# Kernel optimization log

Hardware: AMD Instinct MI355X
Metric: run time of the kernel (lower is better)

The kernel has to match this reference:

```python
import jax, jax.numpy as jnp
import numpy as np

N_HEADS = 16

def setup_inputs() -> dict:
    key = jax.random.key(0)
    k1, k2, k3, k4, k5 = jax.random.split(key, 5)
    B, T, C = 4, 2048, 1024
    x = jax.random.normal(k1, (B, T, C), dtype=jnp.float32)
    W_attn = jax.random.normal(k2, (C, 3 * C), dtype=jnp.float32) * 0.02
    b_attn = jnp.zeros((3 * C,), dtype=jnp.float32)
    W_proj = jax.random.normal(k3, (C, C), dtype=jnp.float32) * 0.02
    b_proj = jnp.zeros((C,), dtype=jnp.float32)
    return {"x": x, "W_attn": W_attn, "b_attn": b_attn, "W_proj": W_proj, "b_proj": b_proj}

def reference(x, W_attn, b_attn, W_proj, b_proj):
    B, T, C = x.shape
    H = N_HEADS
    hd = C // H
    qkv = x @ W_attn + b_attn                      # [B,T,3C]
    q, k, v = jnp.split(qkv, 3, axis=-1)
    q = q.reshape(B, T, H, hd)
    k = k.reshape(B, T, H, hd)
    v = v.reshape(B, T, H, hd)
    scale = 0.1 / jnp.sqrt(jnp.float32(hd))
    scores = jnp.einsum('bqhd,bkhd->bhqk', q, k) * scale   # [B,H,T,T]
    causal = jnp.tril(jnp.ones((T, T), dtype=bool))
    scores = jnp.where(causal[None, None], scores, jnp.float32(-jnp.inf))
    attn = jax.nn.softmax(scores, axis=-1)
    y = jnp.einsum('bhqk,bkhd->bqhd', attn, v).reshape(B, T, C)
    return y @ W_proj + b_proj
```

## Files before the change

kernel.cpp:

```cpp
#include <hip/hip_runtime.h>

typedef __attribute__((ext_vector_type(8))) __bf16 bf16x8;
typedef __attribute__((ext_vector_type(4))) float  f32x4;
typedef __attribute__((ext_vector_type(4))) short  short4v;
typedef __attribute__((ext_vector_type(4))) float  float4v;

#define MFMA16(a,b,c) __builtin_amdgcn_mfma_f32_16x16x32_bf16((a),(b),(c),0,0,0)

__device__ __forceinline__ short f2bf(float f){
    unsigned int u = __builtin_bit_cast(unsigned int, f);
    u += 0x7fffu + ((u >> 16) & 1u);
    return (short)(u >> 16);
}

typedef __attribute__((address_space(1))) void gvoid;
typedef __attribute__((address_space(3))) void lvoid;
__device__ __forceinline__ void async_copy16(const void* g, void* l){
    __builtin_amdgcn_global_load_lds(
        (gvoid*)(unsigned long long)g,
        (lvoid*)(unsigned int)(unsigned long long)l,
        16, 0, 0);
}

#define BATCH 4
#define SEQ   2048
#define CDIM  1024
#define NH    16
#define HD    64
#define BT    8192
#define QSCALE 0.0125f
#define L2E 1.44269504088896340736f

__global__ __launch_bounds__(256) void cvt_x(const float* __restrict__ x,
                                             short* __restrict__ xb){
    int idx = blockIdx.x * 256 + threadIdx.x;
    const float* s = x + (size_t)idx * 8;
    float4v a = *(const float4v*)(s);
    float4v b = *(const float4v*)(s + 4);
    short4v lo, hi;
#pragma unroll
    for (int j = 0; j < 4; ++j){ lo[j] = f2bf(a[j]); hi[j] = f2bf(b[j]); }
    short4v* d = (short4v*)(xb + (size_t)idx * 8);
    d[0] = lo; d[1] = hi;
}

__global__ __launch_bounds__(256) void wtrans(const float* __restrict__ W,
                                              short* __restrict__ Wt,
                                              int K, int N){
    __shared__ __align__(16) short lds[64 * 80];
    int tid = threadIdx.x;
    int n0 = blockIdx.x * 64, k0 = blockIdx.y * 64;
#pragma unroll
    for (int it = 0; it < 4; ++it){
        int idx = it * 256 + tid;
        int r = idx >> 4, c4 = (idx & 15) << 2;
        float4v w = *(const float4v*)(W + (size_t)(k0 + r) * N + n0 + c4);
        short4v h4;
#pragma unroll
        for (int j = 0; j < 4; ++j) h4[j] = f2bf(w[j]);
        *(short4v*)(&lds[r * 80 + c4]) = h4;
    }
    __syncthreads();
#pragma unroll
    for (int it = 0; it < 2; ++it){
        int idx = it * 256 + tid;
        int nl = idx >> 3, k8 = (idx & 7) << 3;
        short4v o0, o1;
#pragma unroll
        for (int j = 0; j < 4; ++j){
            o0[j] = lds[(k8 + j) * 80 + nl];
            o1[j] = lds[(k8 + 4 + j) * 80 + nl];
        }
        short4v* d = (short4v*)(Wt + (size_t)(n0 + nl) * K + k0 + k8);
        d[0] = o0; d[1] = o1;
    }
}

#define BM 128
#define BN 128
#define BK 32
#define KDIM 1024

__global__ __launch_bounds__(256) void qkv_gemm(const short* __restrict__ A,
                                                const short* __restrict__ Bt,
                                                const float* __restrict__ bias,
                                                short* __restrict__ q,
                                                short* __restrict__ k,
                                                short* __restrict__ v){
    __shared__ __align__(16) short As[2][BM * BK];
    __shared__ __align__(16) short Bs[2][BM * BK];
    const int tid = threadIdx.x;
    const int bn = blockIdx.x, bm = blockIdx.y;
    const int lane = tid & 63, wid = tid >> 6;
    const int wr = wid >> 1, wc = wid & 1;
    const int li = lane & 15, g = lane >> 4;
    const int arow0 = bm * BM, brow0 = bn * BN;

    f32x4 acc[4][4];
#pragma unroll
    for (int i = 0; i < 4; ++i)
#pragma unroll
        for (int j = 0; j < 4; ++j) acc[i][j] = f32x4{0.f,0.f,0.f,0.f};

    auto stage = [&](int buf, int kt){
        const short* ga = A  + (size_t)arow0 * KDIM + kt * BK;
        const short* gb = Bt + (size_t)brow0 * KDIM + kt * BK;
#pragma unroll
        for (int h = 0; h < 2; ++h){
            int f = h * 256 + tid;
            int row = f >> 2, kc = (f & 3) << 3;
            async_copy16(ga + (size_t)row * KDIM + kc, &As[buf][f << 3]);
            async_copy16(gb + (size_t)row * KDIM + kc, &Bs[buf][f << 3]);
        }
    };

    stage(0, 0);
    __syncthreads();
    int buf = 0;
    const int KT = KDIM / BK;
    for (int kt = 0; kt < KT; ++kt){
        if (kt + 1 < KT) stage(buf ^ 1, kt + 1);
        bf16x8 af[4], bfr[4];
#pragma unroll
        for (int mi = 0; mi < 4; ++mi)
            af[mi] = *(const bf16x8*)(&As[buf][(wr*64 + mi*16 + li) * BK + g*8]);
#pragma unroll
        for (int ni = 0; ni < 4; ++ni)
            bfr[ni] = *(const bf16x8*)(&Bs[buf][(wc*64 + ni*16 + li) * BK + g*8]);
#pragma unroll
        for (int mi = 0; mi < 4; ++mi)
#pragma unroll
            for (int ni = 0; ni < 4; ++ni)
                acc[mi][ni] = MFMA16(af[mi], bfr[ni], acc[mi][ni]);
        __syncthreads();
        buf ^= 1;
    }

    const int sec = bn >> 3;
    const int h   = ((bn & 7) << 1) | wc;
    short* dst = (sec == 0) ? q : ((sec == 1) ? k : v);
    const float mul = (sec == 0) ? QSCALE : 1.0f;
#pragma unroll
    for (int ni = 0; ni < 4; ++ni){
        int d = ni * 16 + li;
        float bb = bias[bn * 128 + wc * 64 + d];
#pragma unroll
        for (int mi = 0; mi < 4; ++mi){
#pragma unroll
            for (int r = 0; r < 4; ++r){
                int row = arow0 + wr * 64 + mi * 16 + g * 4 + r;
                int b_ = row >> 11, t = row & 2047;
                float val = (acc[mi][ni][r] + bb) * mul;
                dst[(((size_t)(b_ * NH + h)) * SEQ + t) * HD + d] = f2bf(val);
            }
        }
    }
}

__global__ __launch_bounds__(256) void proj_gemm(const short* __restrict__ A,
                                                 const short* __restrict__ Bt,
                                                 const float* __restrict__ bias,
                                                 float* __restrict__ out){
    __shared__ __align__(16) short As[2][BM * BK];
    __shared__ __align__(16) short Bs[2][BM * BK];
    const int tid = threadIdx.x;
    const int bn = blockIdx.x, bm = blockIdx.y;
    const int lane = tid & 63, wid = tid >> 6;
    const int wr = wid >> 1, wc = wid & 1;
    const int li = lane & 15, g = lane >> 4;
    const int arow0 = bm * BM, brow0 = bn * BN;

    f32x4 acc[4][4];
#pragma unroll
    for (int i = 0; i < 4; ++i)
#pragma unroll
        for (int j = 0; j < 4; ++j) acc[i][j] = f32x4{0.f,0.f,0.f,0.f};

    auto stage = [&](int buf, int kt){
        const short* ga = A  + (size_t)arow0 * KDIM + kt * BK;
        const short* gb = Bt + (size_t)brow0 * KDIM + kt * BK;
#pragma unroll
        for (int h = 0; h < 2; ++h){
            int f = h * 256 + tid;
            int row = f >> 2, kc = (f & 3) << 3;
            async_copy16(ga + (size_t)row * KDIM + kc, &As[buf][f << 3]);
            async_copy16(gb + (size_t)row * KDIM + kc, &Bs[buf][f << 3]);
        }
    };

    stage(0, 0);
    __syncthreads();
    int buf = 0;
    const int KT = KDIM / BK;
    for (int kt = 0; kt < KT; ++kt){
        if (kt + 1 < KT) stage(buf ^ 1, kt + 1);
        bf16x8 af[4], bfr[4];
#pragma unroll
        for (int mi = 0; mi < 4; ++mi)
            af[mi] = *(const bf16x8*)(&As[buf][(wr*64 + mi*16 + li) * BK + g*8]);
#pragma unroll
        for (int ni = 0; ni < 4; ++ni)
            bfr[ni] = *(const bf16x8*)(&Bs[buf][(wc*64 + ni*16 + li) * BK + g*8]);
#pragma unroll
        for (int mi = 0; mi < 4; ++mi)
#pragma unroll
            for (int ni = 0; ni < 4; ++ni)
                acc[mi][ni] = MFMA16(af[mi], bfr[ni], acc[mi][ni]);
        __syncthreads();
        buf ^= 1;
    }

#pragma unroll
    for (int ni = 0; ni < 4; ++ni){
        int c = brow0 + wc * 64 + ni * 16 + li;
        float bb = bias[c];
#pragma unroll
        for (int mi = 0; mi < 4; ++mi){
#pragma unroll
            for (int r = 0; r < 4; ++r){
                int row = arow0 + wr * 64 + mi * 16 + g * 4 + r;
                out[(size_t)row * CDIM + c] = acc[mi][ni][r] + bb;
            }
        }
    }
}

__global__ __launch_bounds__(256) void vtrans(const short* __restrict__ v,
                                              short* __restrict__ vt){
    __shared__ __align__(16) short lds[64 * 80];
    int tid = threadIdx.x;
    int t0 = blockIdx.x * 64;
    int bh = blockIdx.y;
    const short* src = v + ((size_t)bh * SEQ + t0) * HD;
#pragma unroll
    for (int it = 0; it < 2; ++it){
        int idx = it * 256 + tid;
        int r = idx >> 3, c8 = (idx & 7) << 3;
        *(bf16x8*)(&lds[r * 80 + c8]) = *(const bf16x8*)(src + (size_t)r * HD + c8);
    }
    __syncthreads();
    short* dst = vt + (size_t)bh * HD * SEQ + t0;
#pragma unroll
    for (int it = 0; it < 2; ++it){
        int idx = it * 256 + tid;
        int dl = idx >> 3, t8 = (idx & 7) << 3;
        short4v o0, o1;
#pragma unroll
        for (int j = 0; j < 4; ++j){
            o0[j] = lds[(t8 + j) * 80 + dl];
            o1[j] = lds[(t8 + 4 + j) * 80 + dl];
        }
        short4v* d = (short4v*)(dst + (size_t)dl * SEQ + t8);
        d[0] = o0; d[1] = o1;
    }
}

__global__ __launch_bounds__(256) void attn_kernel(const short* __restrict__ q,
                                                   const short* __restrict__ kk,
                                                   const short* __restrict__ vt,
                                                   short* __restrict__ y){
    __shared__ __align__(16) char kvs[2][2][8192];
    __shared__ __align__(16) char psm[4 * 2048];
    const int tid = threadIdx.x;
    const int qt = 31 - blockIdx.x;
    const int bh = blockIdx.y;
    const int lane = tid & 63, wid = tid >> 6;
    const int li = lane & 15, g = lane >> 4;
    const int iglob = qt * 64 + wid * 16 + li;

    const short* qp = q + ((size_t)bh * SEQ + iglob) * HD;
    bf16x8 qf0 = *(const bf16x8*)(qp + g * 8);
    bf16x8 qf1 = *(const bf16x8*)(qp + 32 + g * 8);

    char* pbase = psm + wid * 2048 + li * 128;
    const int sw = (li & 7) << 4;

    f32x4 acc[4];
#pragma unroll
    for (int df = 0; df < 4; ++df) acc[df] = f32x4{0.f,0.f,0.f,0.f};
    float m = -3e38f, l = 0.f;

    const short* kbp = kk + (size_t)bh * SEQ * HD;
    const short* vbp = vt + (size_t)bh * HD * SEQ;

    const int c0 = (wid * 2) * 64 + lane;
    const int r0 = c0 >> 3, sg0 = (c0 & 7) ^ (r0 & 7);
    const int c1 = c0 + 64;
    const int r1 = c1 >> 3, sg1 = (c1 & 7) ^ (r1 & 7);

    auto stage = [&](int b, int kt2){
        const int kb2 = kt2 * 64;
        const short* kg = kbp + (size_t)kb2 * HD;
        const short* vg = vbp + kb2;
        char* kd = kvs[b][0];
        char* vd = kvs[b][1];
        async_copy16(kg + r0 * HD + sg0 * 8, kd + c0 * 16);
        async_copy16(kg + r1 * HD + sg1 * 8, kd + c1 * 16);
        async_copy16(vg + (size_t)r0 * SEQ + sg0 * 8, vd + c0 * 16);
        async_copy16(vg + (size_t)r1 * SEQ + sg1 * 8, vd + c1 * 16);
    };

    stage(0, 0);
    asm volatile("s_waitcnt vmcnt(0)" ::: "memory");
    __builtin_amdgcn_s_barrier();
    int buf = 0;
    for (int kt = 0; kt <= qt; ++kt){
        const int kb = kt * 64;
        if (kt < qt) stage(buf ^ 1, kt + 1);

        const char* Kb = kvs[buf][0];
        const char* Vb = kvs[buf][1];

        f32x4 st[4];
#pragma unroll
        for (int kf = 0; kf < 4; ++kf) st[kf] = f32x4{0.f,0.f,0.f,0.f};
#pragma unroll
        for (int kf = 0; kf < 4; ++kf){
            int r = kf * 16 + li;
            bf16x8 k0 = *(const bf16x8*)(Kb + r * 128 + ((g ^ (r & 7)) << 4));
            bf16x8 k1 = *(const bf16x8*)(Kb + r * 128 + (((g + 4) ^ (r & 7)) << 4));
            st[kf] = MFMA16(k0, qf0, st[kf]);
            st[kf] = MFMA16(k1, qf1, st[kf]);
        }
        if (kt == qt){
#pragma unroll
            for (int kf = 0; kf < 4; ++kf)
#pragma unroll
                for (int r = 0; r < 4; ++r)
                    if (kb + kf * 16 + g * 4 + r > iglob) st[kf][r] = -3e38f;
        }
        float pm = -3e38f;
#pragma unroll
        for (int kf = 0; kf < 4; ++kf)
#pragma unroll
            for (int r = 0; r < 4; ++r) pm = fmaxf(pm, st[kf][r]);
        pm = fmaxf(pm, __shfl_xor(pm, 16, 64));
        pm = fmaxf(pm, __shfl_xor(pm, 32, 64));
        float mnew = fmaxf(m, pm);
        float alpha = __builtin_amdgcn_exp2f((m - mnew) * L2E);
        float rs = 0.f;
#pragma unroll
        for (int kf = 0; kf < 4; ++kf){
            short4v pk;
#pragma unroll
            for (int r = 0; r < 4; ++r){
                float p = __builtin_amdgcn_exp2f((st[kf][r] - mnew) * L2E);
                rs += p;
                pk[r] = f2bf(p);
            }
            *(short4v*)(pbase + (((kf << 5) + (g << 3)) ^ sw)) = pk;
        }
        rs += __shfl_xor(rs, 16, 64);
        rs += __shfl_xor(rs, 32, 64);
        l = l * alpha + rs;
        m = mnew;
#pragma unroll
        for (int df = 0; df < 4; ++df) acc[df] *= alpha;

        bf16x8 pb0 = *(const bf16x8*)(pbase + (((g << 4)) ^ sw));
        bf16x8 pb1 = *(const bf16x8*)(pbase + ((64 + (g << 4)) ^ sw));
#pragma unroll
        for (int df = 0; df < 4; ++df){
            int d = df * 16 + li;
            bf16x8 v0 = *(const bf16x8*)(Vb + d * 128 + ((g ^ (d & 7)) << 4));
            bf16x8 v1 = *(const bf16x8*)(Vb + d * 128 + (((g + 4) ^ (d & 7)) << 4));
            acc[df] = MFMA16(v0, pb0, acc[df]);
            acc[df] = MFMA16(v1, pb1, acc[df]);
        }

        asm volatile("s_waitcnt vmcnt(0)" ::: "memory");
        __builtin_amdgcn_s_barrier();
        buf ^= 1;
    }

    float rl = 1.f / l;
    const int b_ = bh >> 4, h = bh & 15;
    short* yp = y + ((size_t)(b_ * SEQ + iglob)) * CDIM + h * HD;
#pragma unroll
    for (int df = 0; df < 4; ++df){
        short4v o;
#pragma unroll
        for (int r = 0; r < 4; ++r) o[r] = f2bf(acc[df][r] * rl);
        *(short4v*)(yp + df * 16 + g * 4) = o;
    }
}

extern "C" void kernel_launch(void* const* d_in, const int* in_sizes, int n_in,
                              void* d_out, int out_size, void* d_ws, size_t ws_size,
                              hipStream_t stream){
    const float* x      = (const float*)d_in[0];
    const float* W_attn = (const float*)d_in[1];
    const float* b_attn = (const float*)d_in[2];
    const float* W_proj = (const float*)d_in[3];
    const float* b_proj = (const float*)d_in[4];
    float* out = (float*)d_out;

    if (ws_size < (size_t)92274688) return;

    char* ws = (char*)d_ws;
    short* Wtp = (short*)(ws);
    short* q   = (short*)(ws + 2097152);
    short* kk  = (short*)(ws + 18874368);
    short* v   = (short*)(ws + 35651584);
    short* vt  = (short*)(ws + 52428800);
    short* xb  = (short*)(ws + 69206016);
    short* y   = xb;
    short* Wta = (short*)(ws + 85983232);

    cvt_x <<<4096, 256, 0, stream>>>(x, xb);
    wtrans<<<dim3(48, 16), 256, 0, stream>>>(W_attn, Wta, 1024, 3072);
    wtrans<<<dim3(16, 16), 256, 0, stream>>>(W_proj, Wtp, 1024, 1024);
    qkv_gemm<<<dim3(24, 64), 256, 0, stream>>>(xb, Wta, b_attn, q, kk, v);
    vtrans<<<dim3(32, 64), 256, 0, stream>>>(v, vt);
    attn_kernel<<<dim3(32, 64), 256, 0, stream>>>(q, kk, vt, y);
    proj_gemm<<<dim3(8, 64), 256, 0, stream>>>(y, Wtp, b_proj, out);
}
```

Measured before the change: 326.6 us.

## Defer softmax rescale, use packed bf16 conversion and MFMA priority hints in attention

The online-softmax inner loop now skips the running-max update and the accumulator rescale whenever no lane's new block max exceeds the old max by more than a threshold, so alpha multiplies are mostly avoided. Exponentials are computed with a single fma per element. The manual round-to-nearest bf16 conversion is replaced by the hardware packed v_cvt_pk_bf16_f32 instruction for both P tiles and the output. s_setprio is raised around the MFMA blocks to favor matrix issue across waves. The deferred rescale lets probabilities exceed 1 by up to e^8, which adds some risk to bf16 precision and overflow headroom.

```diff
diff --git a/kernel.cpp b/kernel.cpp
--- a/kernel.cpp
+++ b/kernel.cpp
@@ -4,6 +4,7 @@
 typedef __attribute__((ext_vector_type(4))) float  f32x4;
 typedef __attribute__((ext_vector_type(4))) short  short4v;
 typedef __attribute__((ext_vector_type(4))) float  float4v;
+typedef __attribute__((ext_vector_type(2))) unsigned int uint2v;
 
 #define MFMA16(a,b,c) __builtin_amdgcn_mfma_f32_16x16x32_bf16((a),(b),(c),0,0,0)
 
@@ -11,6 +12,12 @@
     unsigned int u = __builtin_bit_cast(unsigned int, f);
     u += 0x7fffu + ((u >> 16) & 1u);
     return (short)(u >> 16);
+}
+
+__device__ __forceinline__ unsigned int cvtpk(float a, float b){
+    unsigned int w;
+    asm("v_cvt_pk_bf16_f32 %0, %1, %2" : "=v"(w) : "v"(a), "v"(b));
+    return w;
 }
 
 typedef __attribute__((address_space(1))) void gvoid;
@@ -30,6 +37,7 @@
 #define BT    8192
 #define QSCALE 0.0125f
 #define L2E 1.44269504088896340736f
+#define DEFER_THR 8.0f
 
 __global__ __launch_bounds__(256) void cvt_x(const float* __restrict__ x,
                                              short* __restrict__ xb){
@@ -314,6 +322,7 @@
         f32x4 st[4];
 #pragma unroll
         for (int kf = 0; kf < 4; ++kf) st[kf] = f32x4{0.f,0.f,0.f,0.f};
+        __builtin_amdgcn_s_setprio(1);
 #pragma unroll
         for (int kf = 0; kf < 4; ++kf){
             int r = kf * 16 + li;
@@ -322,6 +331,7 @@
             st[kf] = MFMA16(k0, qf0, st[kf]);
             st[kf] = MFMA16(k1, qf1, st[kf]);
         }
+        __builtin_amdgcn_s_setprio(0);
         if (kt == qt){
 #pragma unroll
             for (int kf = 0; kf < 4; ++kf)
@@ -336,29 +346,33 @@
             for (int r = 0; r < 4; ++r) pm = fmaxf(pm, st[kf][r]);
         pm = fmaxf(pm, __shfl_xor(pm, 16, 64));
         pm = fmaxf(pm, __shfl_xor(pm, 32, 64));
-        float mnew = fmaxf(m, pm);
-        float alpha = __builtin_amdgcn_exp2f((m - mnew) * L2E);
+        if (!__all(pm - m <= DEFER_THR)){
+            float mnew = fmaxf(m, pm);
+            float alpha = __builtin_amdgcn_exp2f((m - mnew) * L2E);
+            l *= alpha;
+#pragma unroll
+            for (int df = 0; df < 4; ++df) acc[df] *= alpha;
+            m = mnew;
+        }
+        const float nmL = -m * L2E;
         float rs = 0.f;
 #pragma unroll
         for (int kf = 0; kf < 4; ++kf){
-            short4v pk;
-#pragma unroll
-            for (int r = 0; r < 4; ++r){
-                float p = __builtin_amdgcn_exp2f((st[kf][r] - mnew) * L2E);
-                rs += p;
-                pk[r] = f2bf(p);
-            }
-            *(short4v*)(pbase + (((kf << 5) + (g << 3)) ^ sw)) = pk;
+            float p0 = __builtin_amdgcn_exp2f(__builtin_fmaf(st[kf][0], L2E, nmL));
+            float p1 = __builtin_amdgcn_exp2f(__builtin_fmaf(st[kf][1], L2E, nmL));
+            float p2 = __builtin_amdgcn_exp2f(__builtin_fmaf(st[kf][2], L2E, nmL));
+            float p3 = __builtin_amdgcn_exp2f(__builtin_fmaf(st[kf][3], L2E, nmL));
+            rs += (p0 + p1) + (p2 + p3);
+            uint2v pk = { cvtpk(p0, p1), cvtpk(p2, p3) };
+            *(uint2v*)(pbase + (((kf << 5) + (g << 3)) ^ sw)) = pk;
         }
         rs += __shfl_xor(rs, 16, 64);
         rs += __shfl_xor(rs, 32, 64);
-        l = l * alpha + rs;
-        m = mnew;
-#pragma unroll
-        for (int df = 0; df < 4; ++df) acc[df] *= alpha;
+        l += rs;
 
         bf16x8 pb0 = *(const bf16x8*)(pbase + (((g << 4)) ^ sw));
         bf16x8 pb1 = *(const bf16x8*)(pbase + ((64 + (g << 4)) ^ sw));
+        __builtin_amdgcn_s_setprio(1);
 #pragma unroll
         for (int df = 0; df < 4; ++df){
             int d = df * 16 + li;
@@ -367,6 +381,7 @@
             acc[df] = MFMA16(v0, pb0, acc[df]);
             acc[df] = MFMA16(v1, pb1, acc[df]);
         }
+        __builtin_amdgcn_s_setprio(0);
 
         asm volatile("s_waitcnt vmcnt(0)" ::: "memory");
         __builtin_amdgcn_s_barrier();
@@ -378,10 +393,9 @@
     short* yp = y + ((size_t)(b_ * SEQ + iglob)) * CDIM + h * HD;
 #pragma unroll
     for (int df = 0; df < 4; ++df){
-        short4v o;
-#pragma unroll
-        for (int r = 0; r < 4; ++r) o[r] = f2bf(acc[df][r] * rl);
-        *(short4v*)(yp + df * 16 + g * 4) = o;
+        uint2v o = { cvtpk(acc[df][0] * rl, acc[df][1] * rl),
+                     cvtpk(acc[df][2] * rl, acc[df][3] * rl) };
+        *(uint2v*)(yp + df * 16 + g * 4) = o;
     }
 }
 
```

Measured after the change: 325.3 us. About the same (-0.4%).
